# Kernel tuning notes

Hardware: AMD Instinct MI355X
Metric: run time of the kernel (lower is better)

## Reference

```python
import jax, jax.numpy as jnp
import numpy as np

N, E, D = 50000, 600000, 128
LN_EPS = 1e-5


def setup_inputs() -> dict:
    key = jax.random.key(0)
    ks = jax.random.split(key, 7)
    s = 1.0 / np.sqrt(D)
    x = jax.random.normal(ks[0], (N, D), dtype=jnp.float32)
    edge_index = jax.random.randint(ks[1], (2, E), 0, N, dtype=jnp.int32)
    Wq = jax.random.normal(ks[2], (D, D), dtype=jnp.float32) * s
    Wk = jax.random.normal(ks[3], (D, D), dtype=jnp.float32) * s
    Wv = jax.random.normal(ks[4], (D, D), dtype=jnp.float32) * s
    Wo = jax.random.normal(ks[5], (D, D), dtype=jnp.float32) * s
    bo = jnp.zeros((D,), dtype=jnp.float32)
    gamma = jnp.ones((D,), dtype=jnp.float32)
    beta = jnp.zeros((D,), dtype=jnp.float32)
    return {"x": x, "edge_index": edge_index, "Wq": Wq, "Wk": Wk,
            "Wv": Wv, "Wo": Wo, "bo": bo, "gamma": gamma, "beta": beta}


def reference(x, edge_index, Wq, Wk, Wv, Wo, bo, gamma, beta):
    src, dst = edge_index[0], edge_index[1]
    # gather endpoint features, project (torch Linear: y = x @ W.T)
    q = x[dst] @ Wq.T                      # [E, D]
    k = x[src] @ Wk.T                      # [E, D]
    v = x[src] @ Wv.T                      # [E, D]
    logits = jnp.sum(q * k, axis=-1, keepdims=True) / np.sqrt(D)  # [E, 1]
    msg = jax.nn.sigmoid(logits) * v       # [E, D]
    agg = jax.ops.segment_sum(msg, dst, num_segments=N)  # scatter-add -> [N, D]
    out = agg @ Wo.T + bo
    h = x + out
    # LayerNorm over last dim
    mu = jnp.mean(h, axis=-1, keepdims=True)
    var = jnp.mean(jnp.square(h - mu), axis=-1, keepdims=True)
    return (h - mu) * jax.lax.rsqrt(var + LN_EPS) * gamma + beta
```

## Files before the change

kernel.cpp:

```cpp
#include <hip/hip_runtime.h>
#include <math.h>


#define BM 64

typedef __attribute__((ext_vector_type(8))) short bfrag;
typedef __attribute__((ext_vector_type(4))) float f32x4;
typedef __attribute__((ext_vector_type(2))) _Float16 half2_t;

__device__ __forceinline__ short f2bf(float f) {
    union { float f; unsigned u; } v; v.f = f;
    unsigned r = v.u + 0x7FFFu + ((v.u >> 16) & 1u);
    return (short)(r >> 16);
}
__device__ __forceinline__ float bf2f(short h) {
    union { unsigned u; float f; } v;
    v.u = ((unsigned)(unsigned short)h) << 16;
    return v.f;
}
__device__ __forceinline__ unsigned short f2h(float f) {
    union { _Float16 h; unsigned short u; } v;
    v.h = (_Float16)f;
    return v.u;
}
__device__ __forceinline__ half2_t u2h2(unsigned u) {
    union { unsigned u; half2_t h; } v;
    v.u = u;
    return v.h;
}

__global__ __launch_bounds__(256) void zero_prep(
    const float* __restrict__ Wq, const float* __restrict__ Wk,
    const float* __restrict__ Wv, const float* __restrict__ Wo,
    short* __restrict__ whi, short* __restrict__ wlo,
    int* __restrict__ hist, int N)
{
    int g = blockIdx.x * 256 + threadIdx.x;
    if (g < N) hist[g] = 0;
    if (g < 65536) {
        const float* Ws[4] = {Wq, Wk, Wv, Wo};
        float f = Ws[g >> 14][g & 16383];
        short h = f2bf(f);
        short l = f2bf(f - bf2f(h));
        whi[g] = h; wlo[g] = l;
    }
}

__global__ __launch_bounds__(256) void qkv_mfma(
    const float* __restrict__ x,
    const short* __restrict__ whi, const short* __restrict__ wlo,
    unsigned short* __restrict__ Qh, unsigned short* __restrict__ KV16, int N)
{
    __shared__ short xs_hi[64][136];
    __shared__ short xs_lo[64][136];

    const int tid = threadIdx.x;
    const int row0 = blockIdx.x * BM;

    #pragma unroll
    for (int i = 0; i < 8; ++i) {
        int idx = tid + 256 * i;
        int r = idx >> 5;
        int c4 = idx & 31;
        int gr = row0 + r;
        float4 val = make_float4(0.f, 0.f, 0.f, 0.f);
        if (gr < N) val = ((const float4*)(x + (size_t)gr * 128))[c4];
        short4 h, l;
        h.x = f2bf(val.x); l.x = f2bf(val.x - bf2f(h.x));
        h.y = f2bf(val.y); l.y = f2bf(val.y - bf2f(h.y));
        h.z = f2bf(val.z); l.z = f2bf(val.z - bf2f(h.z));
        h.w = f2bf(val.w); l.w = f2bf(val.w - bf2f(h.w));
        *((short4*)&xs_hi[r][c4 * 4]) = h;
        *((short4*)&xs_lo[r][c4 * 4]) = l;
    }
    __syncthreads();

    const int wid  = tid >> 6;
    const int lane = tid & 63;
    const int n16  = lane & 15;
    const int quad = lane >> 4;

    #pragma unroll 1
    for (int mat = 0; mat < 3; ++mat) {
        const short* __restrict__ WH = whi + mat * 16384;
        const short* __restrict__ WL = wlo + mat * 16384;
        const f32x4 zero = {0.f, 0.f, 0.f, 0.f};
        f32x4 acc[4][2];
        #pragma unroll
        for (int t = 0; t < 4; ++t) { acc[t][0] = zero; acc[t][1] = zero; }

        #pragma unroll
        for (int kc = 0; kc < 4; ++kc) {
            int k0 = kc * 32 + quad * 8;
            bfrag ah[4], al[4], bh[2], bl[2];
            #pragma unroll
            for (int t = 0; t < 4; ++t) {
                ah[t] = *((const bfrag*)&xs_hi[t * 16 + n16][k0]);
                al[t] = *((const bfrag*)&xs_lo[t * 16 + n16][k0]);
            }
            #pragma unroll
            for (int c = 0; c < 2; ++c) {
                int wr = (wid * 2 + c) * 16 + n16;
                bh[c] = *((const bfrag*)(WH + wr * 128 + k0));
                bl[c] = *((const bfrag*)(WL + wr * 128 + k0));
            }
            #pragma unroll
            for (int t = 0; t < 4; ++t)
                #pragma unroll
                for (int c = 0; c < 2; ++c) {
                    acc[t][c] = __builtin_amdgcn_mfma_f32_16x16x32_bf16(ah[t], bh[c], acc[t][c], 0, 0, 0);
                    acc[t][c] = __builtin_amdgcn_mfma_f32_16x16x32_bf16(al[t], bh[c], acc[t][c], 0, 0, 0);
                    acc[t][c] = __builtin_amdgcn_mfma_f32_16x16x32_bf16(ah[t], bl[c], acc[t][c], 0, 0, 0);
                }
        }
        #pragma unroll
        for (int t = 0; t < 4; ++t)
            #pragma unroll
            for (int r = 0; r < 4; ++r) {
                int grow = row0 + t * 16 + quad * 4 + r;
                if (grow < N) {
                    int c0 = (wid * 2 + 0) * 16 + n16;
                    int c1 = (wid * 2 + 1) * 16 + n16;
                    if (mat == 0) {
                        Qh[(size_t)grow * 128 + c0] = f2h(acc[t][0][r]);
                        Qh[(size_t)grow * 128 + c1] = f2h(acc[t][1][r]);
                    } else {
                        int off = (mat == 2) ? 4 : 0;
                        size_t base = (size_t)grow * 256;
                        KV16[base + (c0 >> 2) * 8 + (c0 & 3) + off] = f2h(acc[t][0][r]);
                        KV16[base + (c1 >> 2) * 8 + (c1 & 3) + off] = f2h(acc[t][1][r]);
                    }
                }
            }
    }
}

__global__ __launch_bounds__(256) void hist_kernel(
    const int* __restrict__ ei, int* __restrict__ hist, int E)
{
    int e = blockIdx.x * blockDim.x + threadIdx.x;
    if (e < E) atomicAdd(&hist[ei[E + e]], 1);
}

#define SCAN_TPB 256
#define SCAN_EPT 4

__global__ __launch_bounds__(SCAN_TPB) void scan_partial(
    const int* __restrict__ hist, int* __restrict__ offs,
    int* __restrict__ blockSums, int N)
{
    __shared__ int sdata[SCAN_TPB];
    int b = blockIdx.x;
    int t = threadIdx.x;
    int base = b * SCAN_TPB * SCAN_EPT + t * SCAN_EPT;
    int v[SCAN_EPT];
    int tot = 0;
    #pragma unroll
    for (int j = 0; j < SCAN_EPT; ++j) {
        int idx = base + j;
        v[j] = (idx < N) ? hist[idx] : 0;
        tot += v[j];
    }
    sdata[t] = tot;
    __syncthreads();
    for (int off = 1; off < SCAN_TPB; off <<= 1) {
        int xv = (t >= off) ? sdata[t - off] : 0;
        __syncthreads();
        sdata[t] += xv;
        __syncthreads();
    }
    int run = sdata[t] - tot;
    #pragma unroll
    for (int j = 0; j < SCAN_EPT; ++j) {
        int idx = base + j;
        if (idx < N) offs[idx] = run;
        run += v[j];
    }
    if (t == SCAN_TPB - 1) blockSums[b] = sdata[t];
}

__global__ __launch_bounds__(256) void scan_blocksums(int* __restrict__ blockSums, int nb)
{
    __shared__ int sdata[256];
    int t = threadIdx.x;
    int orig = (t < nb) ? blockSums[t] : 0;
    sdata[t] = orig;
    __syncthreads();
    for (int off = 1; off < 256; off <<= 1) {
        int xv = (t >= off) ? sdata[t - off] : 0;
        __syncthreads();
        sdata[t] += xv;
        __syncthreads();
    }
    if (t < nb) blockSums[t] = sdata[t] - orig;
}

__global__ __launch_bounds__(256) void scan_add(
    int* __restrict__ offs, int* __restrict__ starts,
    const int* __restrict__ blockSums, int N)
{
    int idx = blockIdx.x * blockDim.x + threadIdx.x;
    if (idx < N) {
        int vv = offs[idx] + blockSums[idx >> 10];
        offs[idx] = vv;
        starts[idx] = vv;
    }
}

__global__ __launch_bounds__(256) void scatter_kernel(
    const int* __restrict__ ei, int* __restrict__ offs,
    int* __restrict__ ssrc, int E)
{
    int e = blockIdx.x * blockDim.x + threadIdx.x;
    if (e < E) {
        int d = ei[E + e];
        int pos = atomicAdd(&offs[d], 1);
        ssrc[pos] = ei[e];
    }
}

#define NA 4
__global__ __launch_bounds__(256) void node_agg(
    const int* __restrict__ ssrc,
    const int* __restrict__ starts,
    const int* __restrict__ endoffs,
    const unsigned short* __restrict__ Qh,
    const unsigned short* __restrict__ KV16,
    float* __restrict__ agg, int N)
{
    int node = blockIdx.x * 4 + (threadIdx.x >> 6);
    int lane = threadIdx.x & 63;
    if (node >= N) return;
    int half = lane >> 5;
    int l = lane & 31;

    int start = starts[node];
    int end = endoffs[node];
    int deg = end - start;
    int len0 = (deg + 1) >> 1;
    int hstart = start + half * len0;
    int hend = half ? end : (start + len0);

    uint2 qw = *((const uint2*)(Qh + (size_t)node * 128 + l * 4));
    half2_t q01 = u2h2(qw.x), q23 = u2h2(qw.y);

    float a0 = 0.f, a1 = 0.f, a2 = 0.f, a3 = 0.f;
    int iters = (len0 + NA - 1) / NA;

    int base = hstart;
    for (int it = 0; it < iters; ++it, base += NA) {
        int s[NA]; bool ok[NA];
        #pragma unroll
        for (int j = 0; j < NA; ++j) {
            int idx = base + j;
            ok[j] = (idx < hend);
            idx = ok[j] ? idx : (hend - 1);
            s[j] = ssrc[idx];
        }
        uint4 w[NA];
        #pragma unroll
        for (int j = 0; j < NA; ++j)
            w[j] = *((const uint4*)(KV16 + (size_t)s[j] * 256 + l * 8));
        float p[NA];
        #pragma unroll
        for (int j = 0; j < NA; ++j) {
            p[j] = __builtin_amdgcn_fdot2(u2h2(w[j].x), q01, 0.f, false);
            p[j] = __builtin_amdgcn_fdot2(u2h2(w[j].y), q23, p[j], false);
        }
        #pragma unroll
        for (int j = 0; j < NA; ++j)
            p[j] += __int_as_float(__builtin_amdgcn_ds_swizzle(__float_as_int(p[j]), 0x041F));
        #pragma unroll
        for (int j = 0; j < NA; ++j)
            p[j] += __int_as_float(__builtin_amdgcn_ds_swizzle(__float_as_int(p[j]), 0x081F));
        #pragma unroll
        for (int j = 0; j < NA; ++j)
            p[j] += __int_as_float(__builtin_amdgcn_ds_swizzle(__float_as_int(p[j]), 0x101F));
        #pragma unroll
        for (int j = 0; j < NA; ++j)
            p[j] += __int_as_float(__builtin_amdgcn_ds_swizzle(__float_as_int(p[j]), 0x201F));
        #pragma unroll
        for (int j = 0; j < NA; ++j)
            p[j] += __int_as_float(__builtin_amdgcn_ds_swizzle(__float_as_int(p[j]), 0x401F));

        #pragma unroll
        for (int j = 0; j < NA; ++j) {
            float c = 1.f / (1.f + __expf(-p[j] * 0.0883883476483184f));
            if (!ok[j]) c = 0.f;
            half2_t v01 = u2h2(w[j].z), v23 = u2h2(w[j].w);
            a0 += c * (float)v01.x; a1 += c * (float)v01.y;
            a2 += c * (float)v23.x; a3 += c * (float)v23.y;
        }
    }
    a0 += __shfl_xor(a0, 32);
    a1 += __shfl_xor(a1, 32);
    a2 += __shfl_xor(a2, 32);
    a3 += __shfl_xor(a3, 32);
    if (half == 0)
        *((float4*)(agg + (size_t)node * 128 + l * 4)) = make_float4(a0, a1, a2, a3);
}

__global__ __launch_bounds__(256) void out_ln_mfma(
    const float* __restrict__ agg,
    const short* __restrict__ whi, const short* __restrict__ wlo,
    const float* __restrict__ bo, const float* __restrict__ x,
    const float* __restrict__ gamma, const float* __restrict__ beta,
    float* __restrict__ out, int N)
{
    __shared__ __align__(16) char smem[64 * 136 * 2 * 2];
    short (*xs_hi)[136] = (short(*)[136])smem;
    short (*xs_lo)[136] = (short(*)[136])(smem + 64 * 136 * 2);
    float (*hs)[132]    = (float(*)[132])smem;

    const int tid = threadIdx.x;
    const int row0 = blockIdx.x * BM;

    #pragma unroll
    for (int i = 0; i < 8; ++i) {
        int idx = tid + 256 * i;
        int r = idx >> 5;
        int c4 = idx & 31;
        int gr = row0 + r;
        float4 val = make_float4(0.f, 0.f, 0.f, 0.f);
        if (gr < N) val = ((const float4*)(agg + (size_t)gr * 128))[c4];
        short4 h, l;
        h.x = f2bf(val.x); l.x = f2bf(val.x - bf2f(h.x));
        h.y = f2bf(val.y); l.y = f2bf(val.y - bf2f(h.y));
        h.z = f2bf(val.z); l.z = f2bf(val.z - bf2f(h.z));
        h.w = f2bf(val.w); l.w = f2bf(val.w - bf2f(h.w));
        *((short4*)&xs_hi[r][c4 * 4]) = h;
        *((short4*)&xs_lo[r][c4 * 4]) = l;
    }
    __syncthreads();

    const int wid  = tid >> 6;
    const int lane = tid & 63;
    const int n16  = lane & 15;
    const int quad = lane >> 4;
    const short* __restrict__ WH = whi + 3 * 16384;
    const short* __restrict__ WL = wlo + 3 * 16384;

    const f32x4 zero = {0.f, 0.f, 0.f, 0.f};
    f32x4 acc[4][2];
    #pragma unroll
    for (int t = 0; t < 4; ++t) { acc[t][0] = zero; acc[t][1] = zero; }

    #pragma unroll
    for (int kc = 0; kc < 4; ++kc) {
        int k0 = kc * 32 + quad * 8;
        bfrag ah[4], al[4], bh[2], bl[2];
        #pragma unroll
        for (int t = 0; t < 4; ++t) {
            ah[t] = *((const bfrag*)&xs_hi[t * 16 + n16][k0]);
            al[t] = *((const bfrag*)&xs_lo[t * 16 + n16][k0]);
        }
        #pragma unroll
        for (int c = 0; c < 2; ++c) {
            int wr = (wid * 2 + c) * 16 + n16;
            bh[c] = *((const bfrag*)(WH + wr * 128 + k0));
            bl[c] = *((const bfrag*)(WL + wr * 128 + k0));
        }
        #pragma unroll
        for (int t = 0; t < 4; ++t)
            #pragma unroll
            for (int c = 0; c < 2; ++c) {
                acc[t][c] = __builtin_amdgcn_mfma_f32_16x16x32_bf16(ah[t], bh[c], acc[t][c], 0, 0, 0);
                acc[t][c] = __builtin_amdgcn_mfma_f32_16x16x32_bf16(al[t], bh[c], acc[t][c], 0, 0, 0);
                acc[t][c] = __builtin_amdgcn_mfma_f32_16x16x32_bf16(ah[t], bl[c], acc[t][c], 0, 0, 0);
            }
    }
    __syncthreads();

    #pragma unroll
    for (int t = 0; t < 4; ++t)
        #pragma unroll
        for (int r = 0; r < 4; ++r) {
            hs[t * 16 + quad * 4 + r][(wid * 2 + 0) * 16 + n16] = acc[t][0][r];
            hs[t * 16 + quad * 4 + r][(wid * 2 + 1) * 16 + n16] = acc[t][1][r];
        }
    __syncthreads();

    {
        int r = tid >> 2;
        int qd = tid & 3;
        int gr = row0 + r;
        float sum = 0.f, sq = 0.f;
        #pragma unroll
        for (int c = 0; c < 32; c += 4) {
            float4 g4 = *((float4*)&hs[r][qd * 32 + c]);
            float4 b4 = *((const float4*)(bo + qd * 32 + c));
            float4 x4 = make_float4(0.f, 0.f, 0.f, 0.f);
            if (gr < N) x4 = *((const float4*)(x + (size_t)gr * 128 + qd * 32 + c));
            float4 h = make_float4(g4.x + b4.x + x4.x, g4.y + b4.y + x4.y,
                                   g4.z + b4.z + x4.z, g4.w + b4.w + x4.w);
            *((float4*)&hs[r][qd * 32 + c]) = h;
            sum += h.x + h.y + h.z + h.w;
            sq += h.x * h.x + h.y * h.y + h.z * h.z + h.w * h.w;
        }
        sum += __shfl_xor(sum, 1); sum += __shfl_xor(sum, 2);
        sq  += __shfl_xor(sq, 1);  sq  += __shfl_xor(sq, 2);
        float mu = sum * (1.f / 128.f);
        float var = sq * (1.f / 128.f) - mu * mu;
        float rs = rsqrtf(var + 1e-5f);
        if (gr < N) {
            #pragma unroll
            for (int c = 0; c < 32; c += 4) {
                float4 h = *((float4*)&hs[r][qd * 32 + c]);
                float4 g = *((const float4*)(gamma + qd * 32 + c));
                float4 b = *((const float4*)(beta + qd * 32 + c));
                float4 o = make_float4((h.x - mu) * rs * g.x + b.x,
                                       (h.y - mu) * rs * g.y + b.y,
                                       (h.z - mu) * rs * g.z + b.z,
                                       (h.w - mu) * rs * g.w + b.w);
                *((float4*)(out + (size_t)gr * 128 + qd * 32 + c)) = o;
            }
        }
    }
}

extern "C" void kernel_launch(void* const* d_in, const int* in_sizes, int n_in,
                              void* d_out, int out_size, void* d_ws, size_t ws_size,
                              hipStream_t stream) {
    const float* x     = (const float*)d_in[0];
    const int*   ei    = (const int*)d_in[1];
    const float* Wq    = (const float*)d_in[2];
    const float* Wk    = (const float*)d_in[3];
    const float* Wv    = (const float*)d_in[4];
    const float* Wo    = (const float*)d_in[5];
    const float* bo    = (const float*)d_in[6];
    const float* gamma = (const float*)d_in[7];
    const float* beta  = (const float*)d_in[8];
    const int N = in_sizes[0] / 128;
    const int E = in_sizes[1] / 2;
    const size_t ND = (size_t)N * 128;

    unsigned short* Qh   = (unsigned short*)d_ws;
    unsigned short* KV16 = Qh + ND;
    float* agg = (float*)(KV16 + 2 * ND);
    int* hist      = (int*)(agg + ND);
    int* offs      = hist + N;
    int* starts    = offs + N;
    int* blockSums = starts + N;
    int* ssrc      = blockSums + 256;
    short* whi     = (short*)(ssrc + E);
    short* wlo     = whi + 4 * 16384;

    const int gzp = ((N > 65536 ? N : 65536) + 255) / 256;
    zero_prep<<<gzp, 256, 0, stream>>>(Wq, Wk, Wv, Wo, whi, wlo, hist, N);

    hist_kernel<<<(E + 255) / 256, 256, 0, stream>>>(ei, hist, E);
    const int nScanBlocks = (N + SCAN_TPB * SCAN_EPT - 1) / (SCAN_TPB * SCAN_EPT);
    scan_partial<<<nScanBlocks, SCAN_TPB, 0, stream>>>(hist, offs, blockSums, N);
    scan_blocksums<<<1, 256, 0, stream>>>(blockSums, nScanBlocks);
    scan_add<<<(N + 255) / 256, 256, 0, stream>>>(offs, starts, blockSums, N);
    scatter_kernel<<<(E + 255) / 256, 256, 0, stream>>>(ei, offs, ssrc, E);

    const int gq = (N + BM - 1) / BM;
    qkv_mfma<<<gq, 256, 0, stream>>>(x, whi, wlo, Qh, KV16, N);

    node_agg<<<(N + 3) / 4, 256, 0, stream>>>(ssrc, starts, offs, Qh, KV16, agg, N);

    out_ln_mfma<<<gq, 256, 0, stream>>>(agg, whi, wlo, bo, x, gamma, beta,
                                        (float*)d_out, N);
}
```

Before: 283.7 us.

## Fuse QKV projections in one pass and stage outputs through LDS for coalesced stores

The QKV projection kernel now computes all three matrices in a single k-loop with 24 accumulators, loading x fragments straight from global memory and splitting them into bf16 hi/lo in registers instead of staging them in shared memory. Outputs are written to an LDS buffer first and then copied out with 16-byte coalesced stores, replacing the scattered 2-byte global stores. Occupancy is hinted with launch_bounds(256,2). The costs are much higher register pressure from the accumulators and 32KB of LDS per block. The qkv kernel is only one of several stages, so its share of total time is limited.

```diff
diff --git a/kernel.cpp b/kernel.cpp
--- a/kernel.cpp
+++ b/kernel.cpp
@@ -46,58 +46,54 @@
     }
 }
 
-__global__ __launch_bounds__(256) void qkv_mfma(
+__global__ __launch_bounds__(256, 2) void qkv_mfma(
     const float* __restrict__ x,
     const short* __restrict__ whi, const short* __restrict__ wlo,
     unsigned short* __restrict__ Qh, unsigned short* __restrict__ KV16, int N)
 {
-    __shared__ short xs_hi[64][136];
-    __shared__ short xs_lo[64][136];
-
-    const int tid = threadIdx.x;
+    __shared__ __align__(16) unsigned short obuf[64 * 256];
+
+    const int tid  = threadIdx.x;
     const int row0 = blockIdx.x * BM;
-
-    #pragma unroll
-    for (int i = 0; i < 8; ++i) {
-        int idx = tid + 256 * i;
-        int r = idx >> 5;
-        int c4 = idx & 31;
-        int gr = row0 + r;
-        float4 val = make_float4(0.f, 0.f, 0.f, 0.f);
-        if (gr < N) val = ((const float4*)(x + (size_t)gr * 128))[c4];
-        short4 h, l;
-        h.x = f2bf(val.x); l.x = f2bf(val.x - bf2f(h.x));
-        h.y = f2bf(val.y); l.y = f2bf(val.y - bf2f(h.y));
-        h.z = f2bf(val.z); l.z = f2bf(val.z - bf2f(h.z));
-        h.w = f2bf(val.w); l.w = f2bf(val.w - bf2f(h.w));
-        *((short4*)&xs_hi[r][c4 * 4]) = h;
-        *((short4*)&xs_lo[r][c4 * 4]) = l;
-    }
-    __syncthreads();
-
     const int wid  = tid >> 6;
     const int lane = tid & 63;
     const int n16  = lane & 15;
     const int quad = lane >> 4;
 
-    #pragma unroll 1
-    for (int mat = 0; mat < 3; ++mat) {
-        const short* __restrict__ WH = whi + mat * 16384;
-        const short* __restrict__ WL = wlo + mat * 16384;
-        const f32x4 zero = {0.f, 0.f, 0.f, 0.f};
-        f32x4 acc[4][2];
-        #pragma unroll
-        for (int t = 0; t < 4; ++t) { acc[t][0] = zero; acc[t][1] = zero; }
-
-        #pragma unroll
-        for (int kc = 0; kc < 4; ++kc) {
-            int k0 = kc * 32 + quad * 8;
-            bfrag ah[4], al[4], bh[2], bl[2];
-            #pragma unroll
-            for (int t = 0; t < 4; ++t) {
-                ah[t] = *((const bfrag*)&xs_hi[t * 16 + n16][k0]);
-                al[t] = *((const bfrag*)&xs_lo[t * 16 + n16][k0]);
-            }
+    const f32x4 zero = {0.f, 0.f, 0.f, 0.f};
+    f32x4 acc[3][4][2];
+    #pragma unroll
+    for (int m = 0; m < 3; ++m)
+        #pragma unroll
+        for (int t = 0; t < 4; ++t) { acc[m][t][0] = zero; acc[m][t][1] = zero; }
+
+    #pragma unroll
+    for (int kc = 0; kc < 4; ++kc) {
+        const int k0 = kc * 32 + quad * 8;
+        bfrag ah[4], al[4];
+        #pragma unroll
+        for (int t = 0; t < 4; ++t) {
+            int grow = row0 + t * 16 + n16;
+            float4 a0 = make_float4(0.f, 0.f, 0.f, 0.f);
+            float4 a1 = make_float4(0.f, 0.f, 0.f, 0.f);
+            if (grow < N) {
+                const float* ap = x + (size_t)grow * 128 + k0;
+                a0 = ((const float4*)ap)[0];
+                a1 = ((const float4*)ap)[1];
+            }
+            float av[8] = {a0.x, a0.y, a0.z, a0.w, a1.x, a1.y, a1.z, a1.w};
+            #pragma unroll
+            for (int j = 0; j < 8; ++j) {
+                short hh = f2bf(av[j]);
+                ah[t][j] = hh;
+                al[t][j] = f2bf(av[j] - bf2f(hh));
+            }
+        }
+        #pragma unroll
+        for (int m = 0; m < 3; ++m) {
+            const short* __restrict__ WH = whi + m * 16384;
+            const short* __restrict__ WL = wlo + m * 16384;
+            bfrag bh[2], bl[2];
             #pragma unroll
             for (int c = 0; c < 2; ++c) {
                 int wr = (wid * 2 + c) * 16 + n16;
@@ -108,30 +104,60 @@
             for (int t = 0; t < 4; ++t)
                 #pragma unroll
                 for (int c = 0; c < 2; ++c) {
-                    acc[t][c] = __builtin_amdgcn_mfma_f32_16x16x32_bf16(ah[t], bh[c], acc[t][c], 0, 0, 0);
-                    acc[t][c] = __builtin_amdgcn_mfma_f32_16x16x32_bf16(al[t], bh[c], acc[t][c], 0, 0, 0);
-                    acc[t][c] = __builtin_amdgcn_mfma_f32_16x16x32_bf16(ah[t], bl[c], acc[t][c], 0, 0, 0);
+                    acc[m][t][c] = __builtin_amdgcn_mfma_f32_16x16x32_bf16(ah[t], bh[c], acc[m][t][c], 0, 0, 0);
+                    acc[m][t][c] = __builtin_amdgcn_mfma_f32_16x16x32_bf16(al[t], bh[c], acc[m][t][c], 0, 0, 0);
+                    acc[m][t][c] = __builtin_amdgcn_mfma_f32_16x16x32_bf16(ah[t], bl[c], acc[m][t][c], 0, 0, 0);
                 }
         }
+    }
+
+    {
+        int c0 = wid * 32 + n16, c1 = c0 + 16;
         #pragma unroll
         for (int t = 0; t < 4; ++t)
             #pragma unroll
             for (int r = 0; r < 4; ++r) {
-                int grow = row0 + t * 16 + quad * 4 + r;
-                if (grow < N) {
-                    int c0 = (wid * 2 + 0) * 16 + n16;
-                    int c1 = (wid * 2 + 1) * 16 + n16;
-                    if (mat == 0) {
-                        Qh[(size_t)grow * 128 + c0] = f2h(acc[t][0][r]);
-                        Qh[(size_t)grow * 128 + c1] = f2h(acc[t][1][r]);
-                    } else {
-                        int off = (mat == 2) ? 4 : 0;
-                        size_t base = (size_t)grow * 256;
-                        KV16[base + (c0 >> 2) * 8 + (c0 & 3) + off] = f2h(acc[t][0][r]);
-                        KV16[base + (c1 >> 2) * 8 + (c1 & 3) + off] = f2h(acc[t][1][r]);
-                    }
-                }
-            }
+                int row = t * 16 + quad * 4 + r;
+                obuf[row * 128 + c0] = f2h(acc[0][t][0][r]);
+                obuf[row * 128 + c1] = f2h(acc[0][t][1][r]);
+            }
+    }
+    __syncthreads();
+    {
+        const uint4* src = (const uint4*)obuf;
+        uint4* dst = (uint4*)(Qh + (size_t)row0 * 128);
+        #pragma unroll
+        for (int i = 0; i < 4; ++i) {
+            int sidx = i * 256 + tid;
+            if (row0 + (sidx >> 4) < N) dst[sidx] = src[sidx];
+        }
+    }
+    __syncthreads();
+
+    {
+        int c0 = wid * 32 + n16, c1 = c0 + 16;
+        int p0 = (c0 >> 2) * 8 + (c0 & 3);
+        int p1 = (c1 >> 2) * 8 + (c1 & 3);
+        #pragma unroll
+        for (int t = 0; t < 4; ++t)
+            #pragma unroll
+            for (int r = 0; r < 4; ++r) {
+                int row = t * 16 + quad * 4 + r;
+                obuf[row * 256 + p0]     = f2h(acc[1][t][0][r]);
+                obuf[row * 256 + p0 + 4] = f2h(acc[2][t][0][r]);
+                obuf[row * 256 + p1]     = f2h(acc[1][t][1][r]);
+                obuf[row * 256 + p1 + 4] = f2h(acc[2][t][1][r]);
+            }
+    }
+    __syncthreads();
+    {
+        const uint4* src = (const uint4*)obuf;
+        uint4* dst = (uint4*)(KV16 + (size_t)row0 * 256);
+        #pragma unroll
+        for (int i = 0; i < 8; ++i) {
+            int sidx = i * 256 + tid;
+            if (row0 + (sidx >> 5) < N) dst[sidx] = src[sidx];
+        }
     }
 }
 
```

Result: faster. 277.5 us (-2.2%).
